# Kernel optimization log

Hardware: AMD Instinct MI355X
Metric: run time of the kernel (lower is better)

## Reference

```python
import jax, jax.numpy as jnp
import numpy as np

B, ZD, E, L, NL = 64, 512, 512, 8192, 1000


def irm(x, Ws, bs):
    # IRMLinear(d, n_layers=2): stack of residual linear blocks x <- x + Linear(x)
    for W, b in zip(Ws, bs):
        x = x + x @ W.T + b
    return x


def setup_inputs() -> dict:
    key = jax.random.key(0)
    ks = jax.random.split(key, 10)
    s = lambda k, sh: (jax.random.normal(k, sh, jnp.float32) * 0.02)
    return dict(
        z=jax.random.normal(ks[0], (B, ZD), jnp.float32),
        y=jax.random.randint(ks[1], (B,), 0, NL),
        W_yemb=s(ks[2], (E, NL)), b_yemb=jnp.zeros((E,), jnp.float32),
        Wy1=s(ks[3], (E, E)), by1=jnp.zeros((E,), jnp.float32),
        Wy2=s(ks[4], (E, E)), by2=jnp.zeros((E,), jnp.float32),
        Wz1=s(ks[5], (ZD, ZD)), bz1=jnp.zeros((ZD,), jnp.float32),
        Wz2=s(ks[6], (ZD, ZD)), bz2=jnp.zeros((ZD,), jnp.float32),
        W_zlat=s(ks[7], (L, ZD)),          # Linear(z_dim, lat_size, bias=False)
        w_proj=s(ks[8], (E,)),             # Linear(embed_size, 1, bias=False)
    )


def reference(z, y, W_yemb, b_yemb, Wy1, by1, Wy2, by2, Wz1, bz1, Wz2, bz2, W_zlat, w_proj):
    # y: int64 class ids -> one-hot via identity embedding_mat
    yembed = jax.nn.one_hot(y, NL, dtype=jnp.float32)            # [B, NL]
    ye = yembed @ W_yemb.T + b_yemb                               # [B, E]
    ye = irm(ye, [Wy1, Wy2], [by1, by2])                          # [B, E]
    zz = irm(z, [Wz1, Wz2], [bz1, bz2])                           # [B, ZD]
    zl = zz @ W_zlat.T                                            # [B, L]
    # bmm(z[:,:,1], ye[:,1,:]) then lat_proj over embed collapses to a
    # per-batch scalar: lat[b,i] = zl[b,i] * (ye[b] . w_proj)  (same math,
    # avoids the [B, L, E] intermediate)
    s_scal = ye @ w_proj                                          # [B]
    return zl * s_scal[:, None]                                   # [B, L]
```

## Files before the change

kernel.cpp:

```cpp
#include <hip/hip_runtime.h>


#define BB 64
#define DD 512
#define LL 8192
#define NLBL 1000
#define PIT 68

__device__ __forceinline__ void matvec_block(int eblk, const float* __restrict__ W,
                                             const float* __restrict__ vin,
                                             float* __restrict__ vout) {
  __shared__ float vl[DD];
  __shared__ float red[256];
  int tid = threadIdx.x;
  vl[tid] = vin[tid];
  vl[tid + 256] = vin[tid + 256];
  __syncthreads();
  int el = tid & 31, jg = tid >> 5;
  int e = eblk * 32 + el;
  float acc = 0.f;
  for (int j = jg; j < DD; j += 8)
    acc += W[j * DD + e] * vl[j];
  red[tid] = acc;
  __syncthreads();
  if (tid < 32) {
    float s = vl[eblk * 32 + tid];
#pragma unroll
    for (int g = 0; g < 8; ++g) s += red[g * 32 + tid];
    vout[eblk * 32 + tid] = s;
  }
}

template <int FIRST>
__device__ __forceinline__ void layer_gemm(int blk, const float* __restrict__ Xg,
                                           const float* __restrict__ P1,
                                           const float* __restrict__ W,
                                           const float* __restrict__ bias,
                                           float* __restrict__ P) {
  __shared__ __align__(16) float Xs[BB][PIT];
  __shared__ __align__(16) float Ws[32][PIT];
  int tid = threadIdx.x;
  int jt = blk >> 3, ks = blk & 7;
  int j0 = jt * 32, k0 = ks * 64;
#pragma unroll
  for (int i = 0; i < 4; ++i) {
    int slot = tid + i * 256, row = slot >> 4, c4 = (slot & 15) * 4;
    float4 v;
    if (FIRST) {
      v = *(const float4*)&Xg[row * DD + k0 + c4];
    } else {
      v = float4{0.f, 0.f, 0.f, 0.f};
#pragma unroll
      for (int s = 0; s < 8; ++s) {
        float4 p = *(const float4*)&P1[(s * BB + row) * DD + k0 + c4];
        v.x += p.x; v.y += p.y; v.z += p.z; v.w += p.w;
      }
    }
    *(float4*)&Xs[row][c4] = v;
  }
#pragma unroll
  for (int i = 0; i < 2; ++i) {
    int slot = tid + i * 256, row = slot >> 4, c4 = (slot & 15) * 4;
    *(float4*)&Ws[row][c4] = *(const float4*)&W[(j0 + row) * DD + k0 + c4];
  }
  __syncthreads();
  int jl = tid & 15, bl = tid >> 4;
  float acc[4][2] = {};
#pragma unroll
  for (int k = 0; k < 64; k += 4) {
    float4 xv[4], wv[2];
#pragma unroll
    for (int i = 0; i < 4; ++i) xv[i] = *(const float4*)&Xs[bl + 16 * i][k];
#pragma unroll
    for (int u = 0; u < 2; ++u) wv[u] = *(const float4*)&Ws[jl + 16 * u][k];
#pragma unroll
    for (int i = 0; i < 4; ++i)
#pragma unroll
      for (int u = 0; u < 2; ++u)
        acc[i][u] += xv[i].x * wv[u].x + xv[i].y * wv[u].y +
                     xv[i].z * wv[u].z + xv[i].w * wv[u].w;
  }
#pragma unroll
  for (int i = 0; i < 4; ++i) {
    int b = bl + 16 * i;
#pragma unroll
    for (int u = 0; u < 2; ++u) {
      int jj = j0 + jl + 16 * u;
      float v = acc[i][u];
      if (ks == 0) {
        float xr;
        if (FIRST) {
          xr = Xg[b * DD + jj];
        } else {
          xr = 0.f;
#pragma unroll
          for (int s = 0; s < 8; ++s) xr += P1[(s * BB + b) * DD + jj];
        }
        v += xr + bias[jj];
      }
      P[(ks * BB + b) * DD + jj] = v;
    }
  }
}

__global__ __launch_bounds__(256) void kA(const float* __restrict__ z,
                                          const float* __restrict__ Wz1,
                                          const float* __restrict__ bz1,
                                          float* __restrict__ P1,
                                          const float* __restrict__ Wy2,
                                          const float* __restrict__ w_proj,
                                          float* __restrict__ u1) {
  int blk = blockIdx.x;
  if (blk < 128) layer_gemm<1>(blk, z, nullptr, Wz1, bz1, P1);
  else           matvec_block(blk - 128, Wy2, w_proj, u1);
}

__global__ __launch_bounds__(256) void kB(const float* __restrict__ P1,
                                          const float* __restrict__ Wz2,
                                          const float* __restrict__ bz2,
                                          float* __restrict__ P2,
                                          const float* __restrict__ Wy1,
                                          const float* __restrict__ u1,
                                          float* __restrict__ u0,
                                          const float* __restrict__ by1,
                                          const float* __restrict__ by2,
                                          const float* __restrict__ w_proj,
                                          float* __restrict__ d2) {
  int blk = blockIdx.x;
  if (blk < 128) {
    layer_gemm<0>(blk, nullptr, P1, Wz2, bz2, P2);
  } else if (blk < 144) {
    matvec_block(blk - 128, Wy1, u1, u0);
  } else {
    __shared__ float red[256];
    int tid = threadIdx.x;
    float p = by1[tid] * u1[tid] + by2[tid] * w_proj[tid] +
              by1[tid + 256] * u1[tid + 256] + by2[tid + 256] * w_proj[tid + 256];
    red[tid] = p;
    __syncthreads();
    if (tid < 64) {
      float s = red[tid] + red[tid + 64] + red[tid + 128] + red[tid + 192];
#pragma unroll
      for (int d = 32; d; d >>= 1) s += __shfl_down(s, d, 64);
      if (tid == 0) d2[0] = s;
    }
  }
}

__global__ __launch_bounds__(256) void kC(const float* __restrict__ P2,
                                          const float* __restrict__ W,
                                          float* __restrict__ P3,
                                          const float* __restrict__ W_yemb,
                                          const float* __restrict__ b_yemb,
                                          const int* __restrict__ y,
                                          const float* __restrict__ u0,
                                          const float* __restrict__ d2,
                                          float* __restrict__ sbv) {
  __shared__ __align__(16) float S[16384 + 4096];
  float* Wsl = S;
  float* Zsl = S + 16384;
  int blk = blockIdx.x;
  int tid = threadIdx.x;
  if (blk >= 256) {
    float* u0l = S;
    u0l[tid] = u0[tid];
    u0l[tid + 256] = u0[tid + 256];
    __syncthreads();
    int bl = tid >> 5, el = tid & 31;
    int b = (blk - 256) * 8 + bl;
    int yb = y[b];
    float acc = 0.f;
    for (int e = el; e < DD; e += 32)
      acc += (W_yemb[(size_t)e * NLBL + yb] + b_yemb[e]) * u0l[e];
#pragma unroll
    for (int d = 16; d; d >>= 1) acc += __shfl_down(acc, d, 32);
    if (el == 0) sbv[b] = acc + d2[0];
    return;
  }
  int ks = blk >> 5, lt = blk & 31;
  int l0 = lt * 256, k0 = ks * 64;
  float4 wreg[16];
#pragma unroll
  for (int i = 0; i < 16; ++i) {
    int slot = tid + i * 256, row = slot >> 4, c4 = (slot & 15) * 4;
    wreg[i] = *(const float4*)&W[(size_t)(l0 + row) * DD + k0 + c4];
  }
#pragma unroll
  for (int i = 0; i < 4; ++i) {
    int slot = tid + i * 256, row = slot >> 4, c4 = slot & 15;
    float4 v = float4{0.f, 0.f, 0.f, 0.f};
#pragma unroll
    for (int s = 0; s < 8; ++s) {
      float4 p = *(const float4*)&P2[(s * BB + row) * DD + k0 + c4 * 4];
      v.x += p.x; v.y += p.y; v.z += p.z; v.w += p.w;
    }
    *(float4*)&Zsl[row * 64 + ((c4 ^ (row & 7)) << 2)] = v;
  }
#pragma unroll
  for (int i = 0; i < 16; ++i) {
    int slot = tid + i * 256, row = slot >> 4, c4 = slot & 15;
    *(float4*)&Wsl[row * 64 + ((c4 ^ (row & 7)) << 2)] = wreg[i];
  }
  __syncthreads();
  int bg = tid & 7, lg = tid >> 3;
  int lg7 = lg & 7;
  float acc[8][8] = {};
#pragma unroll
  for (int k4 = 0; k4 < 16; ++k4) {
    int offz = ((k4 ^ bg) << 2);
    int offw = ((k4 ^ lg7) << 2);
    float4 zv[8], wv[8];
#pragma unroll
    for (int i = 0; i < 8; ++i) zv[i] = *(const float4*)&Zsl[(bg + 8 * i) * 64 + offz];
#pragma unroll
    for (int j = 0; j < 8; ++j) wv[j] = *(const float4*)&Wsl[(lg + 32 * j) * 64 + offw];
#pragma unroll
    for (int i = 0; i < 8; ++i)
#pragma unroll
      for (int j = 0; j < 8; ++j)
        acc[i][j] += zv[i].x * wv[j].x + zv[i].y * wv[j].y +
                     zv[i].z * wv[j].z + zv[i].w * wv[j].w;
  }
  float* base = P3 + (size_t)(lt * 8 + ks) * 16384 + tid;
#pragma unroll
  for (int i = 0; i < 8; ++i)
#pragma unroll
    for (int j = 0; j < 8; ++j)
      base[(i * 8 + j) * 256] = acc[i][j];
}

__global__ __launch_bounds__(256) void kD(const float* __restrict__ P3,
                                          const float* __restrict__ sbv,
                                          float* __restrict__ out) {
  __shared__ __align__(16) float T[8][264];
  int tid = threadIdx.x;
  int i = blockIdx.x >> 5, lt = blockIdx.x & 31;
  int bg = tid & 7, lg = tid >> 3;
  float sv = sbv[bg + 8 * i];
#pragma unroll
  for (int j = 0; j < 8; ++j) {
    float v = 0.f;
#pragma unroll
    for (int ks = 0; ks < 8; ++ks)
      v += P3[(size_t)(lt * 8 + ks) * 16384 + (i * 8 + j) * 256 + tid];
    T[bg][lg + 32 * j] = v * sv;
  }
  __syncthreads();
#pragma unroll
  for (int r = 0; r < 2; ++r) {
    int slot = tid + r * 256;
    int row = slot >> 6, c4 = (slot & 63) * 4;
    float4 v = *(const float4*)&T[row][c4];
    *(float4*)&out[(size_t)(8 * i + row) * LL + lt * 256 + c4] = v;
  }
}

extern "C" void kernel_launch(void* const* d_in, const int* in_sizes, int n_in,
                              void* d_out, int out_size, void* d_ws, size_t ws_size,
                              hipStream_t stream) {
  const float* z      = (const float*)d_in[0];
  const int*   y      = (const int*)  d_in[1];
  const float* W_yemb = (const float*)d_in[2];
  const float* b_yemb = (const float*)d_in[3];
  const float* Wy1    = (const float*)d_in[4];
  const float* by1    = (const float*)d_in[5];
  const float* Wy2    = (const float*)d_in[6];
  const float* by2    = (const float*)d_in[7];
  const float* Wz1    = (const float*)d_in[8];
  const float* bz1    = (const float*)d_in[9];
  const float* Wz2    = (const float*)d_in[10];
  const float* bz2    = (const float*)d_in[11];
  const float* W_zlat = (const float*)d_in[12];
  const float* w_proj = (const float*)d_in[13];

  float* ws = (float*)d_ws;
  float* P1 = ws;
  float* P2 = ws + 262144;
  float* P3 = ws + 524288;
  float* u1 = ws + 4718592;
  float* u0 = ws + 4719104;
  float* sb = ws + 4719616;
  float* d2 = ws + 4719680;
  float* out = (float*)d_out;

  kA<<<144, 256, 0, stream>>>(z, Wz1, bz1, P1, Wy2, w_proj, u1);
  kB<<<145, 256, 0, stream>>>(P1, Wz2, bz2, P2, Wy1, u1, u0, by1, by2, w_proj, d2);
  kC<<<264, 256, 0, stream>>>(P2, W_zlat, P3, W_yemb, b_yemb, y, u0, d2, sb);
  kD<<<256, 256, 0, stream>>>(P3, sb, out);
}
```

Before: 154.1 us.

## Use bf16 MFMA for latent projection GEMM and vectorize split-K reduction

Result: no change. 153.8 us (-0.2%).

```diff
diff --git a/kernel.cpp b/kernel.cpp
--- a/kernel.cpp
+++ b/kernel.cpp
@@ -6,6 +6,14 @@
 #define LL 8192
 #define NLBL 1000
 #define PIT 68
+
+typedef __attribute__((ext_vector_type(8))) short short8;
+typedef __attribute__((ext_vector_type(4))) float f32x4;
+
+__device__ __forceinline__ unsigned short f2bf(float f) {
+  unsigned u = __float_as_uint(f);
+  return (unsigned short)((u + 0x7fffu + ((u >> 16) & 1u)) >> 16);
+}
 
 __device__ __forceinline__ void matvec_block(int eblk, const float* __restrict__ W,
                                              const float* __restrict__ vin,
@@ -156,13 +164,13 @@
                                           const float* __restrict__ u0,
                                           const float* __restrict__ d2,
                                           float* __restrict__ sbv) {
-  __shared__ __align__(16) float S[16384 + 4096];
-  float* Wsl = S;
-  float* Zsl = S + 16384;
+  __shared__ __align__(16) unsigned short LB[(256 + 64) * 64];
+  unsigned short* Bs = LB;
+  unsigned short* As = LB + 256 * 64;
   int blk = blockIdx.x;
   int tid = threadIdx.x;
   if (blk >= 256) {
-    float* u0l = S;
+    float* u0l = (float*)LB;
     u0l[tid] = u0[tid];
     u0l[tid + 256] = u0[tid + 256];
     __syncthreads();
@@ -179,11 +187,13 @@
   }
   int ks = blk >> 5, lt = blk & 31;
   int l0 = lt * 256, k0 = ks * 64;
-  float4 wreg[16];
 #pragma unroll
   for (int i = 0; i < 16; ++i) {
-    int slot = tid + i * 256, row = slot >> 4, c4 = (slot & 15) * 4;
-    wreg[i] = *(const float4*)&W[(size_t)(l0 + row) * DD + k0 + c4];
+    int slot = tid + i * 256, row = slot >> 4, c4 = slot & 15;
+    float4 v = *(const float4*)&W[(size_t)(l0 + row) * DD + k0 + c4 * 4];
+    ushort4 h = {f2bf(v.x), f2bf(v.y), f2bf(v.z), f2bf(v.w)};
+    int g = c4 >> 1, half = c4 & 1;
+    *(ushort4*)&Bs[row * 64 + (((g ^ (row & 7)) << 3) + half * 4)] = h;
   }
 #pragma unroll
   for (int i = 0; i < 4; ++i) {
@@ -194,65 +204,71 @@
       float4 p = *(const float4*)&P2[(s * BB + row) * DD + k0 + c4 * 4];
       v.x += p.x; v.y += p.y; v.z += p.z; v.w += p.w;
     }
-    *(float4*)&Zsl[row * 64 + ((c4 ^ (row & 7)) << 2)] = v;
-  }
-#pragma unroll
-  for (int i = 0; i < 16; ++i) {
-    int slot = tid + i * 256, row = slot >> 4, c4 = slot & 15;
-    *(float4*)&Wsl[row * 64 + ((c4 ^ (row & 7)) << 2)] = wreg[i];
+    ushort4 h = {f2bf(v.x), f2bf(v.y), f2bf(v.z), f2bf(v.w)};
+    int g = c4 >> 1, half = c4 & 1;
+    *(ushort4*)&As[row * 64 + (((g ^ (row & 7)) << 3) + half * 4)] = h;
   }
   __syncthreads();
-  int bg = tid & 7, lg = tid >> 3;
-  int lg7 = lg & 7;
-  float acc[8][8] = {};
-#pragma unroll
-  for (int k4 = 0; k4 < 16; ++k4) {
-    int offz = ((k4 ^ bg) << 2);
-    int offw = ((k4 ^ lg7) << 2);
-    float4 zv[8], wv[8];
-#pragma unroll
-    for (int i = 0; i < 8; ++i) zv[i] = *(const float4*)&Zsl[(bg + 8 * i) * 64 + offz];
-#pragma unroll
-    for (int j = 0; j < 8; ++j) wv[j] = *(const float4*)&Wsl[(lg + 32 * j) * 64 + offw];
-#pragma unroll
-    for (int i = 0; i < 8; ++i)
-#pragma unroll
-      for (int j = 0; j < 8; ++j)
-        acc[i][j] += zv[i].x * wv[j].x + zv[i].y * wv[j].y +
-                     zv[i].z * wv[j].z + zv[i].w * wv[j].w;
-  }
-  float* base = P3 + (size_t)(lt * 8 + ks) * 16384 + tid;
-#pragma unroll
-  for (int i = 0; i < 8; ++i)
-#pragma unroll
-    for (int j = 0; j < 8; ++j)
-      base[(i * 8 + j) * 256] = acc[i][j];
+  int wave = tid >> 6, lane = tid & 63;
+  int quad = lane >> 4, l15 = lane & 15;
+  f32x4 acc[4][4] = {};
+#pragma unroll
+  for (int kstep = 0; kstep < 2; ++kstep) {
+    int g = kstep * 4 + quad;
+    short8 af[4], bf[4];
+#pragma unroll
+    for (int mi = 0; mi < 4; ++mi) {
+      int m = mi * 16 + l15;
+      af[mi] = *(const short8*)&As[m * 64 + ((g ^ (m & 7)) << 3)];
+    }
+#pragma unroll
+    for (int ni = 0; ni < 4; ++ni) {
+      int n = wave * 64 + ni * 16 + l15;
+      bf[ni] = *(const short8*)&Bs[n * 64 + ((g ^ (n & 7)) << 3)];
+    }
+#pragma unroll
+    for (int mi = 0; mi < 4; ++mi)
+#pragma unroll
+      for (int ni = 0; ni < 4; ++ni)
+        acc[mi][ni] = __builtin_amdgcn_mfma_f32_16x16x32_bf16(
+            af[mi], bf[ni], acc[mi][ni], 0, 0, 0);
+  }
+  float* base = P3 + (size_t)(lt * 8 + ks) * 16384;
+#pragma unroll
+  for (int mi = 0; mi < 4; ++mi)
+#pragma unroll
+    for (int ni = 0; ni < 4; ++ni) {
+      int l = wave * 64 + ni * 16 + l15;
+#pragma unroll
+      for (int reg = 0; reg < 4; ++reg) {
+        int b = mi * 16 + quad * 4 + reg;
+        base[b * 256 + l] = acc[mi][ni][reg];
+      }
+    }
 }
 
 __global__ __launch_bounds__(256) void kD(const float* __restrict__ P3,
                                           const float* __restrict__ sbv,
                                           float* __restrict__ out) {
-  __shared__ __align__(16) float T[8][264];
-  int tid = threadIdx.x;
+  int t = threadIdx.x;
   int i = blockIdx.x >> 5, lt = blockIdx.x & 31;
-  int bg = tid & 7, lg = tid >> 3;
-  float sv = sbv[bg + 8 * i];
-#pragma unroll
-  for (int j = 0; j < 8; ++j) {
-    float v = 0.f;
-#pragma unroll
-    for (int ks = 0; ks < 8; ++ks)
-      v += P3[(size_t)(lt * 8 + ks) * 16384 + (i * 8 + j) * 256 + tid];
-    T[bg][lg + 32 * j] = v * sv;
-  }
-  __syncthreads();
-#pragma unroll
-  for (int r = 0; r < 2; ++r) {
-    int slot = tid + r * 256;
-    int row = slot >> 6, c4 = (slot & 63) * 4;
-    float4 v = *(const float4*)&T[row][c4];
-    *(float4*)&out[(size_t)(8 * i + row) * LL + lt * 256 + c4] = v;
-  }
+  int b = i * 8 + (t >> 5);
+  int c = (t & 31) * 8;
+  const float* base = P3 + (size_t)(lt * 8) * 16384 + b * 256 + c;
+  float4 a0 = {0.f, 0.f, 0.f, 0.f}, a1 = {0.f, 0.f, 0.f, 0.f};
+#pragma unroll
+  for (int ks = 0; ks < 8; ++ks) {
+    float4 p = *(const float4*)(base + (size_t)ks * 16384);
+    float4 q = *(const float4*)(base + (size_t)ks * 16384 + 4);
+    a0.x += p.x; a0.y += p.y; a0.z += p.z; a0.w += p.w;
+    a1.x += q.x; a1.y += q.y; a1.z += q.z; a1.w += q.w;
+  }
+  float sv = sbv[b];
+  a0.x *= sv; a0.y *= sv; a0.z *= sv; a0.w *= sv;
+  a1.x *= sv; a1.y *= sv; a1.z *= sv; a1.w *= sv;
+  float* o = out + (size_t)b * LL + lt * 256 + c;
+  *(float4*)o = a0;
+  *(float4*)(o + 4) = a1;
 }
 
 extern "C" void kernel_launch(void* const* d_in, const int* in_sizes, int n_in,
```
